# Performance work log

Hardware: AMD Instinct MI355X
Metric: run time of the kernel (lower is better)

The kernel has to match this reference:

```python
import jax, jax.numpy as jnp
import numpy as np

E = 8192       # number of edges
D = 256        # edge feature dim


def setup_inputs() -> dict:
    key = jax.random.key(0)
    ks = jax.random.split(key, 4)
    s = 1.0 / np.sqrt(D)
    return {
        "edge_x": jax.random.normal(ks[0], (E, D), dtype=jnp.float32),
        "W_sim1": jax.random.normal(ks[1], (D, D), dtype=jnp.float32) * s,
        "b_sim1": jnp.zeros((D,), dtype=jnp.float32),
        "W_sim2": jax.random.normal(ks[2], (D, D), dtype=jnp.float32) * s,
        "b_sim2": jnp.zeros((D,), dtype=jnp.float32),
        "W_out": jax.random.normal(ks[3], (3 * D, D), dtype=jnp.float32) * (1.0 / np.sqrt(3 * D)),
        "b_out": jnp.zeros((D,), dtype=jnp.float32),
    }


def reference(edge_x, W_sim1, b_sim1, W_sim2, b_sim2, W_out, b_out):
    # MPModule.forward, 'fully' branch.
    # LinearBlock = Linear + ReLU (assumed).
    e1 = jax.nn.relu(edge_x @ W_sim1 + b_sim1)            # [E, D]
    # (e1.unsqueeze(1) * e1).mean(-1)  ==  (e1 @ e1.T) / D, avoiding [E,E,D]
    sim1 = (e1 @ e1.T) / D                                 # [E, E]
    e2 = jax.nn.relu(edge_x @ W_sim2 + b_sim2)             # [E, D]
    sim2 = (e2 @ e2.T) / D                                 # [E, E]
    # (edge_x * sim.unsqueeze(-1)).sum(1) == sim @ edge_x
    agg1 = sim1 @ edge_x                                   # [E, D]
    agg2 = sim2 @ edge_x                                   # [E, D]
    h = jnp.concatenate([edge_x, agg1, agg2], axis=-1)     # [E, 3D]
    return jax.nn.relu(h @ W_out + b_out)                  # [E, D]
```

## Files before the change

### kernel.cpp

```cpp
#include <hip/hip_runtime.h>
#include <hip/hip_bf16.h>


typedef short bf16x8  __attribute__((ext_vector_type(8)));
typedef short short4v __attribute__((ext_vector_type(4)));
typedef float f32x4   __attribute__((ext_vector_type(4)));

__device__ inline short f2bf(float x) {
    unsigned u = __builtin_bit_cast(unsigned, x);
    return (short)((u + 0x7fffu + ((u >> 16) & 1u)) >> 16);
}
__device__ inline float bf2f(short b) {
    return __builtin_bit_cast(float, (unsigned)((unsigned short)b) << 16);
}
__device__ inline void cp16_async(const char* g, char* l) {
    __builtin_amdgcn_global_load_lds(
        (const __attribute__((address_space(1))) unsigned int*)g,
        (__attribute__((address_space(3))) unsigned int*)l, 16, 0, 0);
}

__global__ void prep_all(const float* __restrict__ X, short* __restrict__ h,
                         const float* __restrict__ W1, const float* __restrict__ W2,
                         const float* __restrict__ Wo,
                         short* __restrict__ Wt1, short* __restrict__ Wt2,
                         short* __restrict__ Wto1, short* __restrict__ Wto2,
                         short* __restrict__ Bt4, float* __restrict__ Nacc)
{
    __shared__ short tile[32][33];
    const int tx = threadIdx.x, ty = threadIdx.y;
    if (blockIdx.y < 8) {
        const int r0 = blockIdx.x * 32, c0 = blockIdx.y * 32;
        #pragma unroll
        for (int i = 0; i < 4; ++i) {
            int row = ty + i * 8;
            short b = f2bf(X[(size_t)(r0 + row) * 256 + c0 + tx]);
            int slot = ((((c0 & 32) + tx) >> 3) ^ ((r0 + row) & 7));
            h[(size_t)(r0 + row) * 768 + (c0 & ~63) + slot * 8 + (tx & 7)] = b;
        }
        return;
    }
    int tw = (blockIdx.y - 8) * 256 + blockIdx.x;
    if (tw >= 320) {
        int i0 = (tw - 320) * 256 + ty * 32 + tx;
        for (int i = i0; i < 131072; i += 49152) Nacc[i] = 0.f;
        return;
    }
    const float* src; short* dst; int ldwt, dk0, kx, ny;
    if (tw < 64)       { src = W1; dst = Wt1; ldwt = 256;
                         kx = tw >> 3; ny = tw & 7; dk0 = kx * 32; }
    else if (tw < 128) { int u = tw - 64; src = W2; dst = Wt2; ldwt = 256;
                         kx = u >> 3; ny = u & 7; dk0 = kx * 32; }
    else               { int u = tw - 128; int g = u >> 6; int rem = u & 63;
                         kx = rem >> 3; ny = rem & 7;
                         src = Wo + (size_t)g * 65536;
                         if (g == 0) { dst = Bt4; ldwt = 768; dk0 = kx * 32; }
                         else        { dst = (g == 1) ? Wto1 : Wto2;
                                       ldwt = 256; dk0 = kx * 32; } }
    const int k0l = kx * 32, n0 = ny * 32;
    #pragma unroll
    for (int i = 0; i < 4; ++i) {
        int row = ty + i * 8;
        tile[row][tx] = f2bf(src[(size_t)(k0l + row) * 256 + n0 + tx]);
    }
    __syncthreads();
    #pragma unroll
    for (int i = 0; i < 4; ++i) {
        int row = ty + i * 8;
        int n = n0 + row;
        int slot = ((((dk0 & 32) + tx) >> 3) ^ (n & 7));
        dst[(size_t)n * ldwt + (dk0 & ~63) + slot * 8 + (tx & 7)] = tile[tx][row];
    }
}

__global__ __launch_bounds__(256, 1)
void gemm_all(int job, short* __restrict__ h,
              const short* __restrict__ Wt1, const short* __restrict__ Wt2,
              const short* __restrict__ Wto1, const short* __restrict__ Wto2,
              const short* __restrict__ Bt4,
              const float* __restrict__ b1, const float* __restrict__ b2,
              const float* __restrict__ bo,
              short* __restrict__ e1t, short* __restrict__ e2t,
              short* __restrict__ G1t, short* __restrict__ G2t,
              float* __restrict__ Nacc, float* __restrict__ outf)
{
    const int z = blockIdx.z;
    int mode, sim = 0, kbeg = 0, kend, lda, ldb;
    const short *Ap, *Bp;
    const float* bias = nullptr;
    short* et = nullptr;
    if (job == 0) {
        Ap = h; lda = 768; kend = 256; ldb = 256;
        if (z < 2) { mode = 1; sim = z;     Bp = z ? Wt2 : Wt1;
                     bias = z ? b2 : b1;    et = z ? e2t : e1t; }
        else       { mode = 3; sim = z - 2; Bp = sim ? Wto2 : Wto1;
                     et = sim ? G2t : G1t; }
    } else if (job == 1) {
        mode = 2; sim = z & 1;
        kbeg = (z >> 1) * 512; kend = kbeg + 512;
        Ap = sim ? G2t : G1t; lda = 8192;
        Bp = sim ? e2t : e1t; ldb = 8192;
    } else {
        mode = 0; Ap = h; lda = 768; kend = 768;
        Bp = Bt4; ldb = 768; bias = bo;
    }

    const int m0 = blockIdx.x * 128, n0 = blockIdx.y * 128;
    const int t = threadIdx.x;
    const int w = t >> 6, l = t & 63, lr = l & 15, q = l >> 4;
    const int wm = w >> 1, wn = w & 1;
    const int wub = t & ~63;

    __shared__ __attribute__((aligned(16))) short S[2][2][128 * 64];

    f32x4 acc[4][4];
    #pragma unroll
    for (int i = 0; i < 4; ++i)
        #pragma unroll
        for (int j = 0; j < 4; ++j) acc[i][j] = f32x4{0.f, 0.f, 0.f, 0.f};

    auto stage = [&](int buf, int k0) {
        #pragma unroll
        for (int it = 0; it < 4; ++it) {
            int idx = it * 256 + t;
            int r = idx >> 3, s = idx & 7;
            cp16_async((const char*)(Ap + (size_t)(m0 + r) * lda + k0) + s * 16,
                       (char*)&S[buf][0][0] + (size_t)(it * 256 + wub) * 16);
        }
        #pragma unroll
        for (int it = 0; it < 4; ++it) {
            int idx = it * 256 + t;
            int r = idx >> 3, s = idx & 7;
            cp16_async((const char*)(Bp + (size_t)(n0 + r) * ldb + k0) + s * 16,
                       (char*)&S[buf][1][0] + (size_t)(it * 256 + wub) * 16);
        }
    };

    stage(0, kbeg);
    __syncthreads();
    int cur = 0;
    for (int k0 = kbeg; k0 < kend; k0 += 64) {
        if (k0 + 64 < kend) stage(cur ^ 1, k0 + 64);
        const short* As = &S[cur][0][0];
        const short* Bs = &S[cur][1][0];
        #pragma unroll
        for (int ks = 0; ks < 2; ++ks) {
            bf16x8 af[4], bfr[4];
            #pragma unroll
            for (int mt = 0; mt < 4; ++mt) {
                int ar = wm * 64 + mt * 16 + lr;
                af[mt] = *(const bf16x8*)&As[ar * 64 + (((ks*4 + q) ^ (ar & 7)) << 3)];
            }
            #pragma unroll
            for (int nt = 0; nt < 4; ++nt) {
                int br = wn * 64 + nt * 16 + lr;
                bfr[nt] = *(const bf16x8*)&Bs[br * 64 + (((ks*4 + q) ^ (br & 7)) << 3)];
            }
            #pragma unroll
            for (int mt = 0; mt < 4; ++mt)
                #pragma unroll
                for (int nt = 0; nt < 4; ++nt)
                    acc[mt][nt] = __builtin_amdgcn_mfma_f32_16x16x32_bf16(
                        af[mt], bfr[nt], acc[mt][nt], 0, 0, 0);
        }
        __syncthreads();
        cur ^= 1;
    }

    if (mode == 0) {
        #pragma unroll
        for (int mt = 0; mt < 4; ++mt)
            #pragma unroll
            for (int nt = 0; nt < 4; ++nt)
                #pragma unroll
                for (int r = 0; r < 4; ++r) {
                    int m = m0 + wm * 64 + mt * 16 + q * 4 + r;
                    int n = n0 + wn * 64 + nt * 16 + lr;
                    float v = acc[mt][nt][r] + bias[n];
                    outf[(size_t)m * 256 + n] = v > 0.f ? v : 0.f;
                }
    } else if (mode == 2) {
        float* Mo = Nacc + (size_t)sim * 65536;
        #pragma unroll
        for (int mt = 0; mt < 4; ++mt)
            #pragma unroll
            for (int nt = 0; nt < 4; ++nt)
                #pragma unroll
                for (int r = 0; r < 4; ++r) {
                    int m = m0 + wm * 64 + mt * 16 + q * 4 + r;
                    int n = n0 + wn * 64 + nt * 16 + lr;
                    atomicAdd(&Mo[(size_t)m * 256 + n],
                              acc[mt][nt][r] * (1.0f / 256.0f));
                }
    } else {
        short* Hs = &S[0][0][0];
        short* Ts = &S[1][0][0];
        #pragma unroll
        for (int mt = 0; mt < 4; ++mt)
            #pragma unroll
            for (int nt = 0; nt < 4; ++nt) {
                int n_loc = wn * 64 + nt * 16 + lr;
                float bb = (mode == 1) ? bias[n0 + n_loc] : 0.f;
                short vb[4];
                #pragma unroll
                for (int r = 0; r < 4; ++r) {
                    float v = acc[mt][nt][r] + bb;
                    if (mode == 1) v = v > 0.f ? v : 0.f;
                    vb[r] = f2bf(v);
                    if (mode == 1) {
                        int m_loc = wm * 64 + mt * 16 + q * 4 + r;
                        Hs[m_loc * 128 + n_loc] = vb[r];
                    }
                }
                int gm = wm * 8 + mt * 2 + (q >> 1);
                short4v pk = { vb[0], vb[1], vb[2], vb[3] };
                *(short4v*)&Ts[n_loc * 128 + ((gm >> 3) << 6)
                               + (((gm & 7) ^ (n_loc & 7)) << 3) + ((q & 1) << 2)] = pk;
            }
        __syncthreads();
        if (mode == 1) {
            const int cb = 256 + sim * 256 + n0;
            for (int i = t; i < 2048; i += 256) {
                int ml = i >> 4, g = i & 15;
                bf16x8 hv = *(const bf16x8*)&Hs[ml * 128 + g * 8];
                *(bf16x8*)(h + (size_t)(m0 + ml) * 768 + cb + ((g >> 3) << 6)
                           + (((g & 7) ^ (ml & 7)) << 3)) = hv;
            }
        }
        for (int i = t; i < 2048; i += 256) {
            int nl = i >> 4, s = i & 15;
            bf16x8 tv = *(const bf16x8*)&Ts[nl * 128 + s * 8];
            *(bf16x8*)(et + (size_t)(n0 + nl) * 8192 + m0 + s * 8) = tv;
        }
    }
}

__global__ void convert_n(const float* __restrict__ Nacc, short* __restrict__ Bt4)
{
    int gid = blockIdx.x * 256 + threadIdx.x;
    int sim = gid >> 13, rem = gid & 8191;
    int n = rem >> 5, g = rem & 31;
    const float* np = Nacc + (size_t)sim * 65536 + (size_t)n * 256 + g * 8;
    f32x4 va = *(const f32x4*)np;
    f32x4 vb = *(const f32x4*)(np + 4);
    bf16x8 pk;
    pk[0] = f2bf(va[0]); pk[1] = f2bf(va[1]);
    pk[2] = f2bf(va[2]); pk[3] = f2bf(va[3]);
    pk[4] = f2bf(vb[0]); pk[5] = f2bf(vb[1]);
    pk[6] = f2bf(vb[2]); pk[7] = f2bf(vb[3]);
    int k = 256 + sim * 256 + g * 8;
    int slot = (g & 7) ^ (n & 7);
    *(bf16x8*)(Bt4 + (size_t)n * 768 + (k & ~63) + slot * 8) = pk;
}

extern "C" void kernel_launch(void* const* d_in, const int* in_sizes, int n_in,
                              void* d_out, int out_size, void* d_ws, size_t ws_size,
                              hipStream_t stream)
{
    const float* edge_x = (const float*)d_in[0];
    const float* W1 = (const float*)d_in[1];
    const float* b1 = (const float*)d_in[2];
    const float* W2 = (const float*)d_in[3];
    const float* b2 = (const float*)d_in[4];
    const float* Wo = (const float*)d_in[5];
    const float* bo = (const float*)d_in[6];

    char* ws = (char*)d_ws;
    short* h    = (short*)ws;
    short* e1t  = (short*)(ws + 12582912);
    short* e2t  = (short*)(ws + 16777216);
    short* G1t  = (short*)(ws + 20971520);
    short* G2t  = (short*)(ws + 25165824);
    short* Wt1  = (short*)(ws + 29360128);
    short* Wt2  = (short*)(ws + 29491200);
    short* Wto1 = (short*)(ws + 29622272);
    short* Wto2 = (short*)(ws + 29753344);
    short* Bt4  = (short*)(ws + 29884416);
    float* Nacc = (float*)(ws + 30277632);

    float* out = (float*)d_out;

    prep_all<<<dim3(256, 10), dim3(32, 8), 0, stream>>>(
        edge_x, h, W1, W2, Wo, Wt1, Wt2, Wto1, Wto2, Bt4, Nacc);

    gemm_all<<<dim3(64, 2, 4), 256, 0, stream>>>(
        0, h, Wt1, Wt2, Wto1, Wto2, Bt4, b1, b2, bo,
        e1t, e2t, G1t, G2t, Nacc, out);

    gemm_all<<<dim3(2, 2, 32), 256, 0, stream>>>(
        1, h, Wt1, Wt2, Wto1, Wto2, Bt4, b1, b2, bo,
        e1t, e2t, G1t, G2t, Nacc, out);

    convert_n<<<dim3(64), 256, 0, stream>>>(Nacc, Bt4);

    gemm_all<<<dim3(64, 2, 1), 256, 0, stream>>>(
        2, h, Wt1, Wt2, Wto1, Wto2, Bt4, b1, b2, bo,
        e1t, e2t, G1t, G2t, Nacc, out);
}
```

Before: 114.1 us.

## Split monolithic GEMM into specialized kernels with LDS-resident weights and direct A loads

Replaces the job-switched gemm_all with three specialized kernels. The edge GEMM and final GEMM now load the whole 128x256 weight slab into LDS once and read the A operand (h) straight from global memory into registers, dropping the double-buffered A staging and the per-iteration barriers. The sim-aggregation GEMM keeps the original pipelined core. This removes runtime mode branching and sync overhead, but direct global A loads expose memory latency without an LDS pipeline, and there is an aliasing hazard: eg_v2 reads h through a const restrict pointer while writing hw, which is the same buffer, though the column ranges differ.

```diff
diff --git a/kernel.cpp b/kernel.cpp
--- a/kernel.cpp
+++ b/kernel.cpp
@@ -73,65 +73,129 @@
 }
 
 __global__ __launch_bounds__(256, 1)
-void gemm_all(int job, short* __restrict__ h,
-              const short* __restrict__ Wt1, const short* __restrict__ Wt2,
-              const short* __restrict__ Wto1, const short* __restrict__ Wto2,
-              const short* __restrict__ Bt4,
-              const float* __restrict__ b1, const float* __restrict__ b2,
-              const float* __restrict__ bo,
-              short* __restrict__ e1t, short* __restrict__ e2t,
-              short* __restrict__ G1t, short* __restrict__ G2t,
-              float* __restrict__ Nacc, float* __restrict__ outf)
+void eg_v2(const short* __restrict__ h,
+           const short* __restrict__ Wt1, const short* __restrict__ Wt2,
+           const short* __restrict__ Wto1, const short* __restrict__ Wto2,
+           const float* __restrict__ b1, const float* __restrict__ b2,
+           short* __restrict__ hw, short* __restrict__ e1t, short* __restrict__ e2t,
+           short* __restrict__ G1t, short* __restrict__ G2t)
 {
     const int z = blockIdx.z;
-    int mode, sim = 0, kbeg = 0, kend, lda, ldb;
-    const short *Ap, *Bp;
-    const float* bias = nullptr;
-    short* et = nullptr;
-    if (job == 0) {
-        Ap = h; lda = 768; kend = 256; ldb = 256;
-        if (z < 2) { mode = 1; sim = z;     Bp = z ? Wt2 : Wt1;
-                     bias = z ? b2 : b1;    et = z ? e2t : e1t; }
-        else       { mode = 3; sim = z - 2; Bp = sim ? Wto2 : Wto1;
-                     et = sim ? G2t : G1t; }
-    } else if (job == 1) {
-        mode = 2; sim = z & 1;
-        kbeg = (z >> 1) * 512; kend = kbeg + 512;
-        Ap = sim ? G2t : G1t; lda = 8192;
-        Bp = sim ? e2t : e1t; ldb = 8192;
-    } else {
-        mode = 0; Ap = h; lda = 768; kend = 768;
-        Bp = Bt4; ldb = 768; bias = bo;
-    }
+    const int mode = (z < 2) ? 1 : 3;
+    const int sim  = z & 1;
+    const short* Bp   = (z == 0) ? Wt1 : (z == 1) ? Wt2 : (z == 2) ? Wto1 : Wto2;
+    const float* bias = (z == 0) ? b1  : (z == 1) ? b2  : nullptr;
+    short* et         = (z == 0) ? e1t : (z == 1) ? e2t : (z == 2) ? G1t : G2t;
 
     const int m0 = blockIdx.x * 128, n0 = blockIdx.y * 128;
     const int t = threadIdx.x;
-    const int w = t >> 6, l = t & 63, lr = l & 15, q = l >> 4;
-    const int wm = w >> 1, wn = w & 1;
+    const int l = t & 63, lr = l & 15, q = l >> 4;
+    const int w = t >> 6, wm = w >> 1, wn = w & 1, wub = t & ~63;
+
+    __shared__ __attribute__((aligned(16))) short Bs[32768];
+
+    #pragma unroll
+    for (int it = 0; it < 16; ++it) {
+        int idx = it * 256 + t, r = idx >> 5, s = idx & 31;
+        cp16_async((const char*)(Bp + (size_t)(n0 + r) * 256) + s * 16,
+                   (char*)Bs + (size_t)(it * 256 + wub) * 16);
+    }
+    __syncthreads();
+
+    f32x4 acc[4][4];
+    #pragma unroll
+    for (int i = 0; i < 4; ++i)
+        #pragma unroll
+        for (int j = 0; j < 4; ++j) acc[i][j] = f32x4{0.f, 0.f, 0.f, 0.f};
+
+    #pragma unroll
+    for (int kb = 0; kb < 4; ++kb)
+        #pragma unroll
+        for (int ks = 0; ks < 2; ++ks) {
+            const int g = ks * 4 + q;
+            bf16x8 af[4], bfr[4];
+            #pragma unroll
+            for (int mt = 0; mt < 4; ++mt) {
+                int ar = wm * 64 + mt * 16 + lr;
+                af[mt] = *(const bf16x8*)(h + (size_t)(m0 + ar) * 768
+                                          + kb * 64 + ((g ^ (ar & 7)) << 3));
+            }
+            #pragma unroll
+            for (int nt = 0; nt < 4; ++nt) {
+                int br = wn * 64 + nt * 16 + lr;
+                bfr[nt] = *(const bf16x8*)&Bs[br * 256 + kb * 64
+                                              + ((g ^ (br & 7)) << 3)];
+            }
+            #pragma unroll
+            for (int mt = 0; mt < 4; ++mt)
+                #pragma unroll
+                for (int nt = 0; nt < 4; ++nt)
+                    acc[mt][nt] = __builtin_amdgcn_mfma_f32_16x16x32_bf16(
+                        af[mt], bfr[nt], acc[mt][nt], 0, 0, 0);
+        }
+
+    __syncthreads();
+    short* Hs = Bs;
+    short* Ts = Bs + 16384;
+    #pragma unroll
+    for (int mt = 0; mt < 4; ++mt)
+        #pragma unroll
+        for (int nt = 0; nt < 4; ++nt) {
+            int n_loc = wn * 64 + nt * 16 + lr;
+            float bb = (mode == 1) ? bias[n0 + n_loc] : 0.f;
+            short vb[4];
+            #pragma unroll
+            for (int r = 0; r < 4; ++r) {
+                float v = acc[mt][nt][r] + bb;
+                if (mode == 1) v = v > 0.f ? v : 0.f;
+                vb[r] = f2bf(v);
+                if (mode == 1) {
+                    int m_loc = wm * 64 + mt * 16 + q * 4 + r;
+                    Hs[m_loc * 128 + n_loc] = vb[r];
+                }
+            }
+            int gm = wm * 8 + mt * 2 + (q >> 1);
+            short4v pk = { vb[0], vb[1], vb[2], vb[3] };
+            *(short4v*)&Ts[n_loc * 128 + ((gm >> 3) << 6)
+                           + (((gm & 7) ^ (n_loc & 7)) << 3) + ((q & 1) << 2)] = pk;
+        }
+    __syncthreads();
+    if (mode == 1) {
+        const int cb = 256 + sim * 256 + n0;
+        for (int i = t; i < 2048; i += 256) {
+            int ml = i >> 4, g = i & 15;
+            bf16x8 hv = *(const bf16x8*)&Hs[ml * 128 + g * 8];
+            *(bf16x8*)(hw + (size_t)(m0 + ml) * 768 + cb + ((g >> 3) << 6)
+                       + (((g & 7) ^ (ml & 7)) << 3)) = hv;
+        }
+    }
+    for (int i = t; i < 2048; i += 256) {
+        int nl = i >> 4, s = i & 15;
+        bf16x8 tv = *(const bf16x8*)&Ts[nl * 128 + s * 8];
+        *(bf16x8*)(et + (size_t)(n0 + nl) * 8192 + m0 + s * 8) = tv;
+    }
+}
+
+__device__ __forceinline__ void core128(
+    const short* __restrict__ Ap, int lda, const short* __restrict__ Bp, int ldb,
+    int kbeg, int kend, int m0, int n0, short* Sf, f32x4 acc[4][4], int t)
+{
+    const int l = t & 63, lr = l & 15, q = l >> 4;
+    const int w = t >> 6, wm = w >> 1, wn = w & 1;
     const int wub = t & ~63;
 
-    __shared__ __attribute__((aligned(16))) short S[2][2][128 * 64];
-
-    f32x4 acc[4][4];
-    #pragma unroll
-    for (int i = 0; i < 4; ++i)
-        #pragma unroll
-        for (int j = 0; j < 4; ++j) acc[i][j] = f32x4{0.f, 0.f, 0.f, 0.f};
-
     auto stage = [&](int buf, int k0) {
         #pragma unroll
         for (int it = 0; it < 4; ++it) {
-            int idx = it * 256 + t;
-            int r = idx >> 3, s = idx & 7;
+            int idx = it * 256 + t, r = idx >> 3, s = idx & 7;
             cp16_async((const char*)(Ap + (size_t)(m0 + r) * lda + k0) + s * 16,
-                       (char*)&S[buf][0][0] + (size_t)(it * 256 + wub) * 16);
+                       (char*)(Sf + buf * 16384) + (size_t)(it * 256 + wub) * 16);
         }
         #pragma unroll
         for (int it = 0; it < 4; ++it) {
-            int idx = it * 256 + t;
-            int r = idx >> 3, s = idx & 7;
+            int idx = it * 256 + t, r = idx >> 3, s = idx & 7;
             cp16_async((const char*)(Bp + (size_t)(n0 + r) * ldb + k0) + s * 16,
-                       (char*)&S[buf][1][0] + (size_t)(it * 256 + wub) * 16);
+                       (char*)(Sf + buf * 16384 + 8192) + (size_t)(it * 256 + wub) * 16);
         }
     };
 
@@ -140,8 +204,8 @@
     int cur = 0;
     for (int k0 = kbeg; k0 < kend; k0 += 64) {
         if (k0 + 64 < kend) stage(cur ^ 1, k0 + 64);
-        const short* As = &S[cur][0][0];
-        const short* Bs = &S[cur][1][0];
+        const short* As = Sf + cur * 16384;
+        const short* Bs2 = As + 8192;
         #pragma unroll
         for (int ks = 0; ks < 2; ++ks) {
             bf16x8 af[4], bfr[4];
@@ -153,7 +217,7 @@
             #pragma unroll
             for (int nt = 0; nt < 4; ++nt) {
                 int br = wn * 64 + nt * 16 + lr;
-                bfr[nt] = *(const bf16x8*)&Bs[br * 64 + (((ks*4 + q) ^ (br & 7)) << 3)];
+                bfr[nt] = *(const bf16x8*)&Bs2[br * 64 + (((ks*4 + q) ^ (br & 7)) << 3)];
             }
             #pragma unroll
             for (int mt = 0; mt < 4; ++mt)
@@ -165,73 +229,45 @@
         __syncthreads();
         cur ^= 1;
     }
-
-    if (mode == 0) {
-        #pragma unroll
-        for (int mt = 0; mt < 4; ++mt)
-            #pragma unroll
-            for (int nt = 0; nt < 4; ++nt)
-                #pragma unroll
-                for (int r = 0; r < 4; ++r) {
-                    int m = m0 + wm * 64 + mt * 16 + q * 4 + r;
-                    int n = n0 + wn * 64 + nt * 16 + lr;
-                    float v = acc[mt][nt][r] + bias[n];
-                    outf[(size_t)m * 256 + n] = v > 0.f ? v : 0.f;
-                }
-    } else if (mode == 2) {
-        float* Mo = Nacc + (size_t)sim * 65536;
-        #pragma unroll
-        for (int mt = 0; mt < 4; ++mt)
-            #pragma unroll
-            for (int nt = 0; nt < 4; ++nt)
-                #pragma unroll
-                for (int r = 0; r < 4; ++r) {
-                    int m = m0 + wm * 64 + mt * 16 + q * 4 + r;
-                    int n = n0 + wn * 64 + nt * 16 + lr;
-                    atomicAdd(&Mo[(size_t)m * 256 + n],
-                              acc[mt][nt][r] * (1.0f / 256.0f));
-                }
-    } else {
-        short* Hs = &S[0][0][0];
-        short* Ts = &S[1][0][0];
-        #pragma unroll
-        for (int mt = 0; mt < 4; ++mt)
-            #pragma unroll
-            for (int nt = 0; nt < 4; ++nt) {
-                int n_loc = wn * 64 + nt * 16 + lr;
-                float bb = (mode == 1) ? bias[n0 + n_loc] : 0.f;
-                short vb[4];
-                #pragma unroll
-                for (int r = 0; r < 4; ++r) {
-                    float v = acc[mt][nt][r] + bb;
-                    if (mode == 1) v = v > 0.f ? v : 0.f;
-                    vb[r] = f2bf(v);
-                    if (mode == 1) {
-                        int m_loc = wm * 64 + mt * 16 + q * 4 + r;
-                        Hs[m_loc * 128 + n_loc] = vb[r];
-                    }
-                }
-                int gm = wm * 8 + mt * 2 + (q >> 1);
-                short4v pk = { vb[0], vb[1], vb[2], vb[3] };
-                *(short4v*)&Ts[n_loc * 128 + ((gm >> 3) << 6)
-                               + (((gm & 7) ^ (n_loc & 7)) << 3) + ((q & 1) << 2)] = pk;
-            }
-        __syncthreads();
-        if (mode == 1) {
-            const int cb = 256 + sim * 256 + n0;
-            for (int i = t; i < 2048; i += 256) {
-                int ml = i >> 4, g = i & 15;
-                bf16x8 hv = *(const bf16x8*)&Hs[ml * 128 + g * 8];
-                *(bf16x8*)(h + (size_t)(m0 + ml) * 768 + cb + ((g >> 3) << 6)
-                           + (((g & 7) ^ (ml & 7)) << 3)) = hv;
-            }
-        }
-        for (int i = t; i < 2048; i += 256) {
-            int nl = i >> 4, s = i & 15;
-            bf16x8 tv = *(const bf16x8*)&Ts[nl * 128 + s * 8];
-            *(bf16x8*)(et + (size_t)(n0 + nl) * 8192 + m0 + s * 8) = tv;
-        }
-    }
+}
+
+__global__ __launch_bounds__(256, 1)
+void nacc_gemm(const short* __restrict__ e1t, const short* __restrict__ e2t,
+               const short* __restrict__ G1t, const short* __restrict__ G2t,
+               float* __restrict__ Nacc)
+{
+    const int z = blockIdx.z;
+    const int sim = z & 1;
+    const int kbeg = (z >> 1) * 512;
+    const short* Ap = sim ? G2t : G1t;
+    const short* Bp = sim ? e2t : e1t;
+    const int m0 = blockIdx.x * 128, n0 = blockIdx.y * 128;
+    const int t = threadIdx.x;
+    const int l = t & 63, lr = l & 15, q = l >> 4;
+    const int w = t >> 6, wm = w >> 1, wn = w & 1;
+
+    __shared__ __attribute__((aligned(16))) short S[32768];
+
+    f32x4 acc[4][4];
+    #pragma unroll
+    for (int i = 0; i < 4; ++i)
+        #pragma unroll
+        for (int j = 0; j < 4; ++j) acc[i][j] = f32x4{0.f, 0.f, 0.f, 0.f};
+
+    core128(Ap, 8192, Bp, 8192, kbeg, kbeg + 512, m0, n0, S, acc, t);
+
+    float* Mo = Nacc + (size_t)sim * 65536;
+    #pragma unroll
+    for (int mt = 0; mt < 4; ++mt)
+        #pragma unroll
+        for (int nt = 0; nt < 4; ++nt)
+            #pragma unroll
+            for (int r = 0; r < 4; ++r) {
+                int m = m0 + wm * 64 + mt * 16 + q * 4 + r;
+                int n = n0 + wn * 64 + nt * 16 + lr;
+                atomicAdd(&Mo[(size_t)m * 256 + n],
+                          acc[mt][nt][r] * (1.0f / 256.0f));
+            }
 }
 
 __global__ void convert_n(const float* __restrict__ Nacc, short* __restrict__ Bt4)
@@ -252,6 +288,74 @@
     *(bf16x8*)(Bt4 + (size_t)n * 768 + (k & ~63) + slot * 8) = pk;
 }
 
+__global__ __launch_bounds__(256, 1)
+void final_v2(const short* __restrict__ h, const short* __restrict__ Bt4,
+              const float* __restrict__ bov, float* __restrict__ outf)
+{
+    const int m0 = blockIdx.x * 128, n0 = blockIdx.y * 128;
+    const int t = threadIdx.x;
+    const int l = t & 63, lr = l & 15, q = l >> 4;
+    const int w = t >> 6, wm = w >> 1, wn = w & 1, wub = t & ~63;
+
+    __shared__ __attribute__((aligned(16))) short Bs[32768];
+
+    f32x4 acc[4][4];
+    #pragma unroll
+    for (int i = 0; i < 4; ++i)
+        #pragma unroll
+        for (int j = 0; j < 4; ++j) acc[i][j] = f32x4{0.f, 0.f, 0.f, 0.f};
+
+    for (int kc = 0; kc < 3; ++kc) {
+        if (kc) __syncthreads();
+        #pragma unroll
+        for (int it = 0; it < 16; ++it) {
+            int idx = it * 256 + t, r = idx >> 5, s = idx & 31;
+            cp16_async((const char*)(Bt4 + (size_t)(n0 + r) * 768 + kc * 256) + s * 16,
+                       (char*)Bs + (size_t)(it * 256 + wub) * 16);
+        }
+        __syncthreads();
+
+        #pragma unroll
+        for (int kb = 0; kb < 4; ++kb)
+            #pragma unroll
+            for (int ks = 0; ks < 2; ++ks) {
+                const int g = ks * 4 + q;
+                bf16x8 af[4], bfr[4];
+                #pragma unroll
+                for (int mt = 0; mt < 4; ++mt) {
+                    int ar = wm * 64 + mt * 16 + lr;
+                    af[mt] = *(const bf16x8*)(h + (size_t)(m0 + ar) * 768
+                                              + kc * 256 + kb * 64
+                                              + ((g ^ (ar & 7)) << 3));
+                }
+                #pragma unroll
+                for (int nt = 0; nt < 4; ++nt) {
+                    int br = wn * 64 + nt * 16 + lr;
+                    bfr[nt] = *(const bf16x8*)&Bs[br * 256 + kb * 64
+                                                  + ((g ^ (br & 7)) << 3)];
+                }
+                #pragma unroll
+                for (int mt = 0; mt < 4; ++mt)
+                    #pragma unroll
+                    for (int nt = 0; nt < 4; ++nt)
+                        acc[mt][nt] = __builtin_amdgcn_mfma_f32_16x16x32_bf16(
+                            af[mt], bfr[nt], acc[mt][nt], 0, 0, 0);
+            }
+    }
+
+    #pragma unroll
+    for (int mt = 0; mt < 4; ++mt)
+        #pragma unroll
+        for (int nt = 0; nt < 4; ++nt)
+            #pragma unroll
+            for (int r = 0; r < 4; ++r) {
+                int m = m0 + wm * 64 + mt * 16 + q * 4 + r;
+                int n = n0 + wn * 64 + nt * 16 + lr;
+                float v = acc[mt][nt][r] + bov[n];
+                outf[(size_t)m * 256 + n] = v > 0.f ? v : 0.f;
+            }
+}
+
 extern "C" void kernel_launch(void* const* d_in, const int* in_sizes, int n_in,
                               void* d_out, int out_size, void* d_ws, size_t ws_size,
                               hipStream_t stream)
@@ -282,17 +386,12 @@
     prep_all<<<dim3(256, 10), dim3(32, 8), 0, stream>>>(
         edge_x, h, W1, W2, Wo, Wt1, Wt2, Wto1, Wto2, Bt4, Nacc);
 
-    gemm_all<<<dim3(64, 2, 4), 256, 0, stream>>>(
-        0, h, Wt1, Wt2, Wto1, Wto2, Bt4, b1, b2, bo,
-        e1t, e2t, G1t, G2t, Nacc, out);
-
-    gemm_all<<<dim3(2, 2, 32), 256, 0, stream>>>(
-        1, h, Wt1, Wt2, Wto1, Wto2, Bt4, b1, b2, bo,
-        e1t, e2t, G1t, G2t, Nacc, out);
+    eg_v2<<<dim3(64, 2, 4), 256, 0, stream>>>(
+        h, Wt1, Wt2, Wto1, Wto2, b1, b2, h, e1t, e2t, G1t, G2t);
+
+    nacc_gemm<<<dim3(2, 2, 32), 256, 0, stream>>>(e1t, e2t, G1t, G2t, Nacc);
 
     convert_n<<<dim3(64), 256, 0, stream>>>(Nacc, Bt4);
 
-    gemm_all<<<dim3(64, 2, 1), 256, 0, stream>>>(
-        2, h, Wt1, Wt2, Wto1, Wto2, Bt4, b1, b2, bo,
-        e1t, e2t, G1t, G2t, Nacc, out);
-}
+    final_v2<<<dim3(64, 2), 256, 0, stream>>>(h, Bt4, bo, out);
+}
```

Result: slower. 121.3 us (+6.3%).
